# Kernel optimization log

Measured on AMD Instinct MI355X. Metric: run time of the kernel, lower is better.

## Reference

```python
import jax, jax.numpy as jnp
import numpy as np

N = 4096
C = 256
H = 8
D = C // H
E = 65536
MAX_DIST = 4
MAX_DEG = 32
FF_MULT = 2
EPS = 1e-5


def _layer_norm(x, gamma, beta):
    mu = jnp.mean(x, axis=-1, keepdims=True)
    var = jnp.mean(jnp.square(x - mu), axis=-1, keepdims=True)
    return (x - mu) * jax.lax.rsqrt(var + EPS) * gamma + beta


def _shortest_path_buckets(edge_index, num_nodes, max_distance):
    far = max_distance + 1
    row, col = edge_index[0], edge_index[1]
    adj = jnp.zeros((num_nodes, num_nodes), dtype=bool)
    adj = adj.at[row, col].set(True).at[col, row].set(True)
    ids = jnp.arange(num_nodes)
    dist = jnp.full((num_nodes, num_nodes), far, dtype=jnp.int32)
    dist = dist.at[ids, ids].set(0)
    seen = jnp.eye(num_nodes, dtype=bool)
    frontier = adj
    adj_i = adj.astype(jnp.int32)
    for d in range(1, max_distance + 1):  # small fixed loop (max_distance=4)
        frontier = frontier & ~seen
        dist = jnp.where(frontier, jnp.int32(d), dist)
        seen = seen | frontier
        frontier = (frontier.astype(jnp.int32) @ adj_i) > 0
    return dist


def setup_inputs() -> dict:
    key = jax.random.key(0)
    ks = jax.random.split(key, 16)
    s = 0.02
    inp = {
        'x': jax.random.normal(ks[0], (N, C), jnp.float32),
        'edge_index': jax.random.randint(ks[1], (2, E), 0, N, jnp.int64),
        'deg_emb': jax.random.normal(ks[2], (MAX_DEG + 2, C), jnp.float32) * s,
        'spa_emb': jax.random.normal(ks[3], (MAX_DIST + 2, H), jnp.float32) * s,
        'Wq': jax.random.normal(ks[4], (C, C), jnp.float32) * s,
        'bq': jnp.zeros((C,), jnp.float32),
        'Wk': jax.random.normal(ks[5], (C, C), jnp.float32) * s,
        'bk': jnp.zeros((C,), jnp.float32),
        'Wv': jax.random.normal(ks[6], (C, C), jnp.float32) * s,
        'bv': jnp.zeros((C,), jnp.float32),
        'Wo': jax.random.normal(ks[7], (C, C), jnp.float32) * s,
        'bo': jnp.zeros((C,), jnp.float32),
        'g1': jnp.ones((C,), jnp.float32),
        'b1': jnp.zeros((C,), jnp.float32),
        'g2': jnp.ones((C,), jnp.float32),
        'b2': jnp.zeros((C,), jnp.float32),
        'Wf1': jax.random.normal(ks[8], (C, FF_MULT * C), jnp.float32) * s,
        'bf1': jnp.zeros((FF_MULT * C,), jnp.float32),
        'Wf2': jax.random.normal(ks[9], (FF_MULT * C, C), jnp.float32) * s,
        'bf2': jnp.zeros((C,), jnp.float32),
    }
    return inp


def _forward(x, edge_index, deg_emb, spa_emb, Wq, bq, Wk, bk, Wv, bv, Wo, bo,
             g1, b1, g2, b2, Wf1, bf1, Wf2, bf2):
    num_nodes = x.shape[0]
    row, col = edge_index[0], edge_index[1]
    # degree: in+out degree, clamped to max_degree+1
    deg = jnp.zeros((num_nodes,), jnp.int32).at[row].add(1).at[col].add(1)
    deg = jnp.minimum(deg, MAX_DEG + 1)
    hidden = x + deg_emb[deg]
    q = (hidden @ Wq + bq).reshape(num_nodes, H, D)
    k = (hidden @ Wk + bk).reshape(num_nodes, H, D)
    v = (hidden @ Wv + bv).reshape(num_nodes, H, D)
    scores = jnp.einsum('nhd,mhd->hnm', q, k) / jnp.sqrt(jnp.float32(D))
    dist = _shortest_path_buckets(edge_index, num_nodes, MAX_DIST)  # [N, N] int
    bias = spa_emb[dist].transpose(2, 0, 1)  # [H, N, N]
    attn = jax.nn.softmax(scores + bias, axis=-1)
    attended = jnp.einsum('hnm,mhd->nhd', attn, v).reshape(num_nodes, C)
    attended = attended @ Wo + bo
    h = _layer_norm(x + attended, g1, b1)
    ff = jax.nn.gelu(h @ Wf1 + bf1, approximate=False) @ Wf2 + bf2
    return _layer_norm(h + ff, g2, b2)


def reference(x, edge_index, deg_emb, spa_emb, Wq, bq, Wk, bk, Wv, bv, Wo, bo,
              g1, b1, g2, b2, Wf1, bf1, Wf2, bf2):
    return _forward(x, edge_index, deg_emb, spa_emb, Wq, bq, Wk, bk, Wv, bv,
                    Wo, bo, g1, b1, g2, b2, Wf1, bf1, Wf2, bf2)
```

## Files before the change

kernel.cpp:

```cpp
#include <hip/hip_runtime.h>
#include <math.h>

#define NN 4096
#define CC 256
#define HH 8
#define DD 32
#define EE 65536

typedef unsigned short u16;
typedef unsigned int u32;
typedef unsigned long long u64;
typedef unsigned char u8;

typedef float f32x4 __attribute__((ext_vector_type(4)));
typedef __bf16 bf16x8 __attribute__((ext_vector_type(8)));

__device__ __forceinline__ u16 f2b(float f){
  u32 u = __float_as_uint(f);
  return (u16)((u + 0x7FFFu + ((u >> 16) & 1u)) >> 16);
}
__device__ __forceinline__ u32 pk2(float a, float b){
  u32 r; asm("v_cvt_pk_bf16_f32 %0,%1,%2" : "=v"(r) : "v"(a), "v"(b)); return r;
}

__global__ __launch_bounds__(256) void k_deg(const int* __restrict__ ei, int* __restrict__ deg){
  int e = blockIdx.x * 256 + threadIdx.x;
  if (e < EE){
    atomicAdd(&deg[ei[e]], 1);
    atomicAdd(&deg[ei[EE + e]], 1);
  }
}

__global__ __launch_bounds__(256) void k_scan(const int* __restrict__ deg, int* __restrict__ rowp,
                                              int* __restrict__ cur){
  __shared__ int part[256];
  int t = threadIdx.x;
  int local[16];
  int s = 0;
  #pragma unroll
  for (int i = 0; i < 16; i++){ local[i] = s; s += deg[t*16 + i]; }
  part[t] = s;
  __syncthreads();
  for (int off = 1; off < 256; off <<= 1){
    int v = (t >= off) ? part[t - off] : 0;
    __syncthreads();
    part[t] += v;
    __syncthreads();
  }
  int excl = (t == 0) ? 0 : part[t - 1];
  #pragma unroll
  for (int i = 0; i < 16; i++){ int v = excl + local[i]; rowp[t*16+i] = v; cur[t*16+i] = v; }
  if (t == 255) rowp[4096] = excl + s;
}

__global__ __launch_bounds__(256) void k_fill(const int* __restrict__ ei, int* __restrict__ cur,
                                              int* __restrict__ col){
  int e = blockIdx.x * 256 + threadIdx.x;
  if (e < EE){
    int r = ei[e], c = ei[EE + e];
    col[atomicAdd(&cur[r], 1)] = c;
    col[atomicAdd(&cur[c], 1)] = r;
  }
}

__global__ __launch_bounds__(256) void k_hidden(const float* __restrict__ x, const float* __restrict__ demb,
                                                const int* __restrict__ deg, u16* __restrict__ hb){
  int i = blockIdx.x * 256 + threadIdx.x;
  int n = i >> 8, c = i & 255;
  int d = deg[n]; if (d > 33) d = 33;
  hb[i] = f2b(x[i] + demb[d * CC + c]);
}

__global__ __launch_bounds__(256) void k_b0(u64* __restrict__ B0){
  int i = blockIdx.x * 256 + threadIdx.x;
  int j = i >> 6, w = i & 63;
  B0[i] = (w == (j >> 6)) ? (1ull << (j & 63)) : 0ull;
}

__global__ __launch_bounds__(256) void k_prop(const u64* __restrict__ Bp, u64* __restrict__ Bn,
                                              const int* __restrict__ rowp, const int* __restrict__ col){
  int i = blockIdx.x * 256 + threadIdx.x;
  int j = i >> 6, w = i & 63;
  u64 acc = Bp[i];
  int s = rowp[j], e = rowp[j + 1];
  u64 a0 = 0, a1 = 0, a2 = 0, a3 = 0;
  int p = s;
  for (; p + 4 <= e; p += 4){
    int c0 = col[p], c1 = col[p+1], c2 = col[p+2], c3 = col[p+3];
    a0 |= Bp[(c0 << 6) + w];
    a1 |= Bp[(c1 << 6) + w];
    a2 |= Bp[(c2 << 6) + w];
    a3 |= Bp[(c3 << 6) + w];
  }
  for (; p < e; p++) a0 |= Bp[(col[p] << 6) + w];
  Bn[i] = acc | (a0 | a1) | (a2 | a3);
}

__global__ __launch_bounds__(256) void k_dist(const u64* __restrict__ B1, const u64* __restrict__ B2,
                                              const u64* __restrict__ B3, const u64* __restrict__ B4,
                                              u8* __restrict__ dist){
  int i = blockIdx.x * 256 + threadIdx.x;
  int j = i >> 6, w = i & 63;
  u64 b1 = B1[i], b2 = B2[i], b3 = B3[i], b4 = B4[i];
  u32 ob[16];
  #pragma unroll
  for (int g = 0; g < 16; g++){
    u32 word = 0;
    #pragma unroll
    for (int q = 0; q < 4; q++){
      int bit = g * 4 + q;
      u32 d;
      if ((b1 >> bit) & 1) d = 1;
      else if ((b2 >> bit) & 1) d = 2;
      else if ((b3 >> bit) & 1) d = 3;
      else if ((b4 >> bit) & 1) d = 4;
      else d = 5;
      if ((w << 6) + bit == j) d = 0;
      word |= d << (q * 8);
    }
    ob[g] = word;
  }
  uint4* dp = (uint4*)(dist + ((size_t)j << 12) + (w << 6));
  uint4* ov = (uint4*)ob;
  dp[0] = ov[0]; dp[1] = ov[1]; dp[2] = ov[2]; dp[3] = ov[3];
}

__global__ __launch_bounds__(256) void k_tconv(const float* __restrict__ W0, const float* __restrict__ W1,
                                               const float* __restrict__ W2, const float* __restrict__ W3,
                                               const float* __restrict__ W4, const float* __restrict__ W5,
                                               u16* __restrict__ T0, u16* __restrict__ T1,
                                               u16* __restrict__ T2, u16* __restrict__ T3,
                                               u16* __restrict__ T4, u16* __restrict__ T5){
  __shared__ float Ts[64][65];
  int z = blockIdx.z;
  const float* W; u16* T; int K, N;
  switch (z){
    case 0: W = W0; T = T0; K = 256; N = 256; break;
    case 1: W = W1; T = T1; K = 256; N = 256; break;
    case 2: W = W2; T = T2; K = 256; N = 256; break;
    case 3: W = W3; T = T3; K = 256; N = 256; break;
    case 4: W = W4; T = T4; K = 256; N = 512; break;
    default: W = W5; T = T5; K = 512; N = 256; break;
  }
  int n0 = blockIdx.x * 64, k0 = blockIdx.y * 64;
  if (n0 >= N || k0 >= K) return;
  int t = threadIdx.x;
  int r = t >> 4, c4 = (t & 15) * 4;
  #pragma unroll
  for (int it = 0; it < 4; it++){
    float4 v = *(const float4*)&W[(size_t)(k0 + it*16 + r) * N + n0 + c4];
    Ts[it*16 + r][c4+0] = v.x; Ts[it*16 + r][c4+1] = v.y;
    Ts[it*16 + r][c4+2] = v.z; Ts[it*16 + r][c4+3] = v.w;
  }
  __syncthreads();
  #pragma unroll
  for (int it = 0; it < 4; it++){
    int n = it*16 + r;
    uint2 o;
    o.x = pk2(Ts[c4+0][n], Ts[c4+1][n]);
    o.y = pk2(Ts[c4+2][n], Ts[c4+3][n]);
    *(uint2*)&T[(size_t)(n0 + n) * K + k0 + c4] = o;
  }
}

__global__ __launch_bounds__(256) void k_bcat(const float* __restrict__ a, const float* __restrict__ b,
                                              const float* __restrict__ c, float* __restrict__ o){
  int i = blockIdx.x * 256 + threadIdx.x;
  if (i < 768){
    float v = (i < 256) ? a[i] : (i < 512) ? b[i - 256] : c[i - 512];
    o[i] = v;
  }
}

__global__ __launch_bounds__(256) void k_gemm32(const u16* __restrict__ A, const u16* __restrict__ Wt,
                                                const float* __restrict__ bias,
                                                float* __restrict__ outF, u16* __restrict__ outB,
                                                u16* __restrict__ outT,
                                                int M, int N, int K, int OS, int mode){
  __shared__ __align__(16) u16 As[32][72];
  __shared__ __align__(16) u16 Bs[64][72];
  int t = threadIdx.x;
  int lane = t & 63;
  int wv = t >> 6;
  int m0 = blockIdx.x * 32, n0 = blockIdx.y * 64;
  int ar = t >> 3, ak = (t & 7) * 8;
  int br = t >> 2, bk = (t & 3) * 16;
  int row16 = lane & 15, kq = (lane >> 4) * 8, rg = (lane >> 4) * 4;
  f32x4 acc0 = {0.f,0.f,0.f,0.f}, acc1 = {0.f,0.f,0.f,0.f};
  for (int k0 = 0; k0 < K; k0 += 64){
    __syncthreads();
    *(bf16x8*)&As[ar][ak]   = *(const bf16x8*)&A [(size_t)(m0 + ar) * K + k0 + ak];
    *(bf16x8*)&Bs[br][bk]   = *(const bf16x8*)&Wt[(size_t)(n0 + br) * K + k0 + bk];
    *(bf16x8*)&Bs[br][bk+8] = *(const bf16x8*)&Wt[(size_t)(n0 + br) * K + k0 + bk + 8];
    __syncthreads();
    #pragma unroll
    for (int ks = 0; ks < 2; ks++){
      bf16x8 a0 = *(const bf16x8*)&As[     row16][ks*32 + kq];
      bf16x8 a1 = *(const bf16x8*)&As[16 + row16][ks*32 + kq];
      bf16x8 b  = *(const bf16x8*)&Bs[wv*16 + row16][ks*32 + kq];
      acc0 = __builtin_amdgcn_mfma_f32_16x16x32_bf16(a0, b, acc0, 0, 0, 0);
      acc1 = __builtin_amdgcn_mfma_f32_16x16x32_bf16(a1, b, acc1, 0, 0, 0);
    }
  }
  int gn = n0 + wv*16 + row16;
  float bv = bias[gn];
  #pragma unroll
  for (int fm = 0; fm < 2; fm++){
    f32x4 aa = fm ? acc1 : acc0;
    #pragma unroll
    for (int r = 0; r < 4; r++){
      int gm = m0 + fm*16 + rg + r;
      float v = aa[r] + bv;
      if (mode & 8) v = 0.5f * v * (1.0f + erff(v * 0.70710678118654752f));
      if (outT && gn >= 512)      outT[(size_t)(gn - 512) * M + gm] = f2b(v);
      else if (mode & 1)          outF[(size_t)gm * N + gn] = v;
      else                        outB[(size_t)gm * OS + gn] = f2b(v);
    }
  }
}

__global__ __launch_bounds__(256) void k_attn(const u16* __restrict__ qg, const u16* __restrict__ kg,
                                              int CS, const u16* __restrict__ vtg,
                                              const u8* __restrict__ dist,
                                              const float* __restrict__ spa,
                                              float* __restrict__ pacc, float* __restrict__ pml){
  __shared__ __align__(16) u16 P[4][32][72];
  __shared__ __align__(16) u8 dls[4][32][72];
  __shared__ float spas[48];
  int t = threadIdx.x;
  int lane = t & 63;
  int wv = t >> 6;
  int h = blockIdx.y * 4 + wv;
  int q0 = blockIdx.x * 32;
  int ck = blockIdx.z;
  int kbase = ck * 1024;
  if (t < 48) spas[t] = spa[t] * 1.4426950408889634f;
  __syncthreads();
  int row16 = lane & 15;
  int kq = (lane >> 4) * 8;
  int rg = (lane >> 4) * 4;
  int hDD = h * DD;
  const char* spasB = (const char*)spas + (h << 2);
  int srow = lane >> 3, scol = (lane & 7) * 8;

  bf16x8 qf0 = *(const bf16x8*)&qg[(size_t)(q0 +      row16) * CS + hDD + kq];
  bf16x8 qf1 = *(const bf16x8*)&qg[(size_t)(q0 + 16 + row16) * CS + hDD + kq];

  const u16* kp0 = kg  + (size_t)(kbase +      row16) * CS + hDD + kq;
  const u16* kp1 = kg  + (size_t)(kbase + 16 + row16) * CS + hDD + kq;
  const u16* kp2 = kg  + (size_t)(kbase + 32 + row16) * CS + hDD + kq;
  const u16* kp3 = kg  + (size_t)(kbase + 48 + row16) * CS + hDD + kq;
  const u16* vp0 = vtg + (size_t)(hDD +      row16) * NN + kbase + kq;
  const u16* vp1 = vtg + (size_t)(hDD + 16 + row16) * NN + kbase + kq;
  const u8*  dp0 = dist + (size_t)(q0 +      srow) * NN + kbase + scol;
  const u8*  dp1 = dist + (size_t)(q0 +  8 + srow) * NN + kbase + scol;
  const u8*  dp2 = dist + (size_t)(q0 + 16 + srow) * NN + kbase + scol;
  const u8*  dp3 = dist + (size_t)(q0 + 24 + srow) * NN + kbase + scol;

  f32x4 zero = {0.f, 0.f, 0.f, 0.f};
  f32x4 acc[2][2] = {{zero, zero}, {zero, zero}};
  float ls[2] = {0.f, 0.f};
  const float scale2 = 0.25506600600499404f;

  uint2 dr0 = *(const uint2*)dp0; dp0 += 64;
  uint2 dr1 = *(const uint2*)dp1; dp1 += 64;
  uint2 dr2 = *(const uint2*)dp2; dp2 += 64;
  uint2 dr3 = *(const uint2*)dp3; dp3 += 64;

  for (int tt = 0; tt < 16; tt++){
    *(uint2*)&dls[wv][     srow][scol] = dr0;
    *(uint2*)&dls[wv][ 8 + srow][scol] = dr1;
    *(uint2*)&dls[wv][16 + srow][scol] = dr2;
    *(uint2*)&dls[wv][24 + srow][scol] = dr3;
    if (tt != 15){
      dr0 = *(const uint2*)dp0; dp0 += 64;
      dr1 = *(const uint2*)dp1; dp1 += 64;
      dr2 = *(const uint2*)dp2; dp2 += 64;
      dr3 = *(const uint2*)dp3; dp3 += 64;
    }
    bf16x8 kf0 = *(const bf16x8*)kp0; kp0 += 64 * 512;
    bf16x8 kf1 = *(const bf16x8*)kp1; kp1 += 64 * 512;
    bf16x8 kf2 = *(const bf16x8*)kp2; kp2 += 64 * 512;
    bf16x8 kf3 = *(const bf16x8*)kp3; kp3 += 64 * 512;
    f32x4 sc[2][4];
    sc[0][0] = __builtin_amdgcn_mfma_f32_16x16x32_bf16(kf0, qf0, zero, 0, 0, 0);
    sc[1][0] = __builtin_amdgcn_mfma_f32_16x16x32_bf16(kf0, qf1, zero, 0, 0, 0);
    sc[0][1] = __builtin_amdgcn_mfma_f32_16x16x32_bf16(kf1, qf0, zero, 0, 0, 0);
    sc[1][1] = __builtin_amdgcn_mfma_f32_16x16x32_bf16(kf1, qf1, zero, 0, 0, 0);
    sc[0][2] = __builtin_amdgcn_mfma_f32_16x16x32_bf16(kf2, qf0, zero, 0, 0, 0);
    sc[1][2] = __builtin_amdgcn_mfma_f32_16x16x32_bf16(kf2, qf1, zero, 0, 0, 0);
    sc[0][3] = __builtin_amdgcn_mfma_f32_16x16x32_bf16(kf3, qf0, zero, 0, 0, 0);
    sc[1][3] = __builtin_amdgcn_mfma_f32_16x16x32_bf16(kf3, qf1, zero, 0, 0, 0);
    #pragma unroll
    for (int fm = 0; fm < 2; fm++){
      int qrow = fm*16 + row16;
      float rs = 0.f;
      #pragma unroll
      for (int fn = 0; fn < 4; fn++){
        u32 dw5 = (*(const u32*)&dls[wv][qrow][fn*16 + rg]) << 5;
        float b0 = *(const float*)(spasB + (dw5 & 255u));
        float b1 = *(const float*)(spasB + ((dw5 >> 8) & 255u));
        float b2 = *(const float*)(spasB + ((dw5 >> 16) & 255u));
        float b3 = *(const float*)(spasB + (dw5 >> 24));
        float p0 = exp2f(fmaf(sc[fm][fn][0], scale2, b0));
        float p1 = exp2f(fmaf(sc[fm][fn][1], scale2, b1));
        float p2 = exp2f(fmaf(sc[fm][fn][2], scale2, b2));
        float p3 = exp2f(fmaf(sc[fm][fn][3], scale2, b3));
        rs += (p0 + p1) + (p2 + p3);
        uint2 pw = { pk2(p0, p1), pk2(p2, p3) };
        *(uint2*)&P[wv][qrow][fn*16 + rg] = pw;
      }
      ls[fm] += rs;
    }
    #pragma unroll
    for (int ks = 0; ks < 2; ks++){
      bf16x8 pa0 = *(const bf16x8*)&P[wv][     row16][ks*32 + kq];
      bf16x8 pa1 = *(const bf16x8*)&P[wv][16 + row16][ks*32 + kq];
      bf16x8 vf0 = *(const bf16x8*)(vp0 + ks*32);
      bf16x8 vf1 = *(const bf16x8*)(vp1 + ks*32);
      acc[0][0] = __builtin_amdgcn_mfma_f32_16x16x32_bf16(pa0, vf0, acc[0][0], 0, 0, 0);
      acc[0][1] = __builtin_amdgcn_mfma_f32_16x16x32_bf16(pa0, vf1, acc[0][1], 0, 0, 0);
      acc[1][0] = __builtin_amdgcn_mfma_f32_16x16x32_bf16(pa1, vf0, acc[1][0], 0, 0, 0);
      acc[1][1] = __builtin_amdgcn_mfma_f32_16x16x32_bf16(pa1, vf1, acc[1][1], 0, 0, 0);
    }
    vp0 += 64; vp1 += 64;
  }
  #pragma unroll
  for (int fm = 0; fm < 2; fm++){
    ls[fm] += __shfl_xor(ls[fm], 16, 64);
    ls[fm] += __shfl_xor(ls[fm], 32, 64);
  }
  size_t base = ((size_t)ck * 8 + h) * 4096 + q0;
  #pragma unroll
  for (int fm = 0; fm < 2; fm++)
    #pragma unroll
    for (int fd = 0; fd < 2; fd++)
      #pragma unroll
      for (int r = 0; r < 4; r++)
        pacc[(base + fm*16 + rg + r) * 32 + fd*16 + row16] = acc[fm][fd][r];
  if ((lane >> 4) == 0){
    #pragma unroll
    for (int fm = 0; fm < 2; fm++)
      pml[base + fm*16 + row16] = ls[fm];
  }
}

__global__ __launch_bounds__(256) void k_merge(const float* __restrict__ pacc,
                                               const float* __restrict__ pml,
                                               u16* __restrict__ attb){
  int row = blockIdx.x;
  int t = threadIdx.x;
  int h = t >> 5, col = t & 31;
  float o = 0.f, L = 0.f;
  #pragma unroll
  for (int c = 0; c < 4; c++){
    size_t base = ((size_t)c * 8 + h) * 4096 + row;
    o += pacc[base * 32 + col];
    L += pml[base];
  }
  attb[(size_t)row * 256 + h * 32 + col] = f2b(o / L);
}

__global__ __launch_bounds__(256) void k_ln(const float* __restrict__ ina, const float* __restrict__ inb,
                                            const float* __restrict__ g, const float* __restrict__ b,
                                            float* __restrict__ outF, u16* __restrict__ outB){
  int t = threadIdx.x;
  int wv = t >> 6, lane = t & 63;
  int row = blockIdx.x * 4 + wv;
  size_t base = (size_t)row * CC + lane * 4;
  float4 xa = *(const float4*)&ina[base];
  float4 xb = *(const float4*)&inb[base];
  float v0 = xa.x + xb.x, v1 = xa.y + xb.y, v2 = xa.z + xb.z, v3 = xa.w + xb.w;
  float s  = v0 + v1 + v2 + v3;
  float s2 = v0*v0 + v1*v1 + v2*v2 + v3*v3;
  #pragma unroll
  for (int m = 1; m < 64; m <<= 1){
    s  += __shfl_xor(s,  m, 64);
    s2 += __shfl_xor(s2, m, 64);
  }
  float mu  = s * (1.0f / 256.0f);
  float var = s2 * (1.0f / 256.0f) - mu * mu;
  float rs  = rsqrtf(var + 1e-5f);
  float4 gv = *(const float4*)&g[lane * 4];
  float4 bv = *(const float4*)&b[lane * 4];
  float o0 = (v0 - mu) * rs * gv.x + bv.x;
  float o1 = (v1 - mu) * rs * gv.y + bv.y;
  float o2 = (v2 - mu) * rs * gv.z + bv.z;
  float o3 = (v3 - mu) * rs * gv.w + bv.w;
  if (outF){ float4 o = {o0, o1, o2, o3}; *(float4*)&outF[base] = o; }
  if (outB){
    outB[base+0] = f2b(o0); outB[base+1] = f2b(o1);
    outB[base+2] = f2b(o2); outB[base+3] = f2b(o3);
  }
}

extern "C" void kernel_launch(void* const* d_in, const int* in_sizes, int n_in,
                              void* d_out, int out_size, void* d_ws, size_t ws_size,
                              hipStream_t stream){
  const float* x    = (const float*)d_in[0];
  const int*   ei   = (const int*)  d_in[1];
  const float* demb = (const float*)d_in[2];
  const float* spa  = (const float*)d_in[3];
  const float* Wq   = (const float*)d_in[4];
  const float* bq   = (const float*)d_in[5];
  const float* Wk   = (const float*)d_in[6];
  const float* bk   = (const float*)d_in[7];
  const float* Wv   = (const float*)d_in[8];
  const float* bv   = (const float*)d_in[9];
  const float* Wo   = (const float*)d_in[10];
  const float* bo   = (const float*)d_in[11];
  const float* g1   = (const float*)d_in[12];
  const float* b1   = (const float*)d_in[13];
  const float* g2   = (const float*)d_in[14];
  const float* b2   = (const float*)d_in[15];
  const float* Wf1  = (const float*)d_in[16];
  const float* bf1  = (const float*)d_in[17];
  const float* Wf2  = (const float*)d_in[18];
  const float* bf2  = (const float*)d_in[19];

  char* ws = (char*)d_ws;
  size_t off = 0;
  auto take = [&](size_t bytes)->char*{
    char* p = ws + off;
    off = (off + bytes + 255) & ~(size_t)255;
    return p;
  };
  int* deg    = (int*)take(4096 * 4);
  int* rowp   = (int*)take(4097 * 4);
  int* cur    = (int*)take(4096 * 4);
  int* col    = (int*)take(131072 * 4);
  u16* hid    = (u16*)take(2097152);
  u16* Wqkvt  = (u16*)take(768 * 256 * 2);
  u16* Wot    = (u16*)take(131072);
  u16* Wf1t   = (u16*)take(262144);
  u16* Wf2t   = (u16*)take(262144);
  float* bcat = (float*)take(768 * 4);
  u16* qkv    = (u16*)take(4194304);
  u16* vt     = (u16*)take(2097152);
  u16* attb   = (u16*)take(2097152);
  char* SC    = take(18 * 1048576);
  u8* dist    = (u8*)take(16777216);
  u64* B[5];
  for (int i = 0; i < 5; i++) B[i] = (u64*)(SC + (size_t)i * 2097152);
  float* pacc    = (float*)SC;
  float* pml     = (float*)(SC + 16777216);
  float* attnout = (float*)SC;
  float* hf      = (float*)(SC + 4194304);
  u16*   hbf     = (u16*)  (SC + 8388608);
  u16*   ff1     = (u16*)  dist;
  float* ff2     = (float*)(dist + 8388608);
  float* outp    = (float*)d_out;

  hipMemsetAsync(deg, 0, 4096 * 4, stream);
  k_deg   <<<256,  256, 0, stream>>>(ei, deg);
  k_scan  <<<1,    256, 0, stream>>>(deg, rowp, cur);
  k_fill  <<<256,  256, 0, stream>>>(ei, cur, col);
  k_hidden<<<4096, 256, 0, stream>>>(x, demb, deg, hid);
  k_b0    <<<1024, 256, 0, stream>>>(B[0]);
  for (int d = 0; d < 4; d++)
    k_prop<<<1024, 256, 0, stream>>>(B[d], B[d + 1], rowp, col);
  k_dist  <<<1024, 256, 0, stream>>>(B[1], B[2], B[3], B[4], dist);

  k_tconv<<<dim3(8, 8, 6), 256, 0, stream>>>(Wq, Wk, Wv, Wo, Wf1, Wf2,
                                             Wqkvt, Wqkvt + 256*256, Wqkvt + 512*256,
                                             Wot, Wf1t, Wf2t);
  k_bcat <<<3, 256, 0, stream>>>(bq, bk, bv, bcat);

  k_gemm32<<<dim3(128, 12), 256, 0, stream>>>(hid, Wqkvt, bcat, nullptr, qkv, vt,
                                              4096, 768, 256, 512, 2);

  k_attn <<<dim3(128, 2, 4), 256, 0, stream>>>(qkv, qkv + 256, 512, vt, dist, spa, pacc, pml);
  k_merge<<<4096, 256, 0, stream>>>(pacc, pml, attb);

  k_gemm32<<<dim3(128, 4), 256, 0, stream>>>(attb, Wot, bo, attnout, nullptr, nullptr,
                                             4096, 256, 256, 256, 1);
  k_ln   <<<1024, 256, 0, stream>>>(x, attnout, g1, b1, hf, hbf);
  k_gemm32<<<dim3(128, 8), 256, 0, stream>>>(hbf, Wf1t, bf1, nullptr, ff1, nullptr,
                                             4096, 512, 256, 512, 2 | 8);
  k_gemm32<<<dim3(128, 4), 256, 0, stream>>>(ff1, Wf2t, bf2, ff2, nullptr, nullptr,
                                             4096, 256, 512, 256, 1);
  k_ln   <<<1024, 256, 0, stream>>>(hf, ff2, g2, b2, outp, nullptr);
}
```

Before: 306.4 us.

## Fold softmax scale into Q, quantize spatial bias to bytes, split keys eight ways

```diff
diff --git a/kernel.cpp b/kernel.cpp
--- a/kernel.cpp
+++ b/kernel.cpp
@@ -18,6 +18,9 @@
 __device__ __forceinline__ u16 f2b(float f){
   u32 u = __float_as_uint(f);
   return (u16)((u + 0x7FFFu + ((u >> 16) & 1u)) >> 16);
+}
+__device__ __forceinline__ float b2f(u16 b){
+  return __uint_as_float(((u32)b) << 16);
 }
 __device__ __forceinline__ u32 pk2(float a, float b){
   u32 r; asm("v_cvt_pk_bf16_f32 %0,%1,%2" : "=v"(r) : "v"(a), "v"(b)); return r;
@@ -212,6 +215,7 @@
       int gm = m0 + fm*16 + rg + r;
       float v = aa[r] + bv;
       if (mode & 8) v = 0.5f * v * (1.0f + erff(v * 0.70710678118654752f));
+      if ((mode & 16) && gn < 256) v *= 0.25506600600499404f;
       if (outT && gn >= 512)      outT[(size_t)(gn - 512) * M + gm] = f2b(v);
       else if (mode & 1)          outF[(size_t)gm * N + gn] = v;
       else                        outB[(size_t)gm * OS + gn] = f2b(v);
@@ -223,25 +227,32 @@
                                               int CS, const u16* __restrict__ vtg,
                                               const u8* __restrict__ dist,
                                               const float* __restrict__ spa,
-                                              float* __restrict__ pacc, float* __restrict__ pml){
+                                              u16* __restrict__ pacc, float* __restrict__ pml){
   __shared__ __align__(16) u16 P[4][32][72];
   __shared__ __align__(16) u8 dls[4][32][72];
-  __shared__ float spas[48];
   int t = threadIdx.x;
   int lane = t & 63;
   int wv = t >> 6;
   int h = blockIdx.y * 4 + wv;
   int q0 = blockIdx.x * 32;
   int ck = blockIdx.z;
-  int kbase = ck * 1024;
-  if (t < 48) spas[t] = spa[t] * 1.4426950408889634f;
-  __syncthreads();
+  int kbase = ck * 512;
   int row16 = lane & 15;
   int kq = (lane >> 4) * 8;
   int rg = (lane >> 4) * 4;
   int hDD = h * DD;
-  const char* spasB = (const char*)spas + (h << 2);
   int srow = lane >> 3, scol = (lane & 7) * 8;
+
+  u32 ub[6];
+  #pragma unroll
+  for (int b = 0; b < 6; b++){
+    float f = fmaf(spa[b * 8 + h], 369.32993046f, 128.5f);
+    int ui = (int)f;
+    ui = ui < 0 ? 0 : (ui > 255 ? 255 : ui);
+    ub[b] = (u32)ui;
+  }
+  u32 B0123 = ub[0] | (ub[1] << 8) | (ub[2] << 16) | (ub[3] << 24);
+  u32 B45   = ub[4] | (ub[5] << 8);
 
   bf16x8 qf0 = *(const bf16x8*)&qg[(size_t)(q0 +      row16) * CS + hDD + kq];
   bf16x8 qf1 = *(const bf16x8*)&qg[(size_t)(q0 + 16 + row16) * CS + hDD + kq];
@@ -260,19 +271,18 @@
   f32x4 zero = {0.f, 0.f, 0.f, 0.f};
   f32x4 acc[2][2] = {{zero, zero}, {zero, zero}};
   float ls[2] = {0.f, 0.f};
-  const float scale2 = 0.25506600600499404f;
 
   uint2 dr0 = *(const uint2*)dp0; dp0 += 64;
   uint2 dr1 = *(const uint2*)dp1; dp1 += 64;
   uint2 dr2 = *(const uint2*)dp2; dp2 += 64;
   uint2 dr3 = *(const uint2*)dp3; dp3 += 64;
 
-  for (int tt = 0; tt < 16; tt++){
+  for (int tt = 0; tt < 8; tt++){
     *(uint2*)&dls[wv][     srow][scol] = dr0;
     *(uint2*)&dls[wv][ 8 + srow][scol] = dr1;
     *(uint2*)&dls[wv][16 + srow][scol] = dr2;
     *(uint2*)&dls[wv][24 + srow][scol] = dr3;
-    if (tt != 15){
+    if (tt != 7){
       dr0 = *(const uint2*)dp0; dp0 += 64;
       dr1 = *(const uint2*)dp1; dp1 += 64;
       dr2 = *(const uint2*)dp2; dp2 += 64;
@@ -297,15 +307,12 @@
       float rs = 0.f;
       #pragma unroll
       for (int fn = 0; fn < 4; fn++){
-        u32 dw5 = (*(const u32*)&dls[wv][qrow][fn*16 + rg]) << 5;
-        float b0 = *(const float*)(spasB + (dw5 & 255u));
-        float b1 = *(const float*)(spasB + ((dw5 >> 8) & 255u));
-        float b2 = *(const float*)(spasB + ((dw5 >> 16) & 255u));
-        float b3 = *(const float*)(spasB + (dw5 >> 24));
-        float p0 = exp2f(fmaf(sc[fm][fn][0], scale2, b0));
-        float p1 = exp2f(fmaf(sc[fm][fn][1], scale2, b1));
-        float p2 = exp2f(fmaf(sc[fm][fn][2], scale2, b2));
-        float p3 = exp2f(fmaf(sc[fm][fn][3], scale2, b3));
+        u32 dw = *(const u32*)&dls[wv][qrow][fn*16 + rg];
+        u32 pb = __builtin_amdgcn_perm(B45, B0123, dw);
+        float p0 = exp2f(fmaf((float)( pb        & 255u), 0.00390625f, sc[fm][fn][0]));
+        float p1 = exp2f(fmaf((float)((pb >>  8) & 255u), 0.00390625f, sc[fm][fn][1]));
+        float p2 = exp2f(fmaf((float)((pb >> 16) & 255u), 0.00390625f, sc[fm][fn][2]));
+        float p3 = exp2f(fmaf((float)( pb >> 24        ), 0.00390625f, sc[fm][fn][3]));
         rs += (p0 + p1) + (p2 + p3);
         uint2 pw = { pk2(p0, p1), pk2(p2, p3) };
         *(uint2*)&P[wv][qrow][fn*16 + rg] = pw;
@@ -337,7 +344,7 @@
     for (int fd = 0; fd < 2; fd++)
       #pragma unroll
       for (int r = 0; r < 4; r++)
-        pacc[(base + fm*16 + rg + r) * 32 + fd*16 + row16] = acc[fm][fd][r];
+        pacc[(base + fm*16 + rg + r) * 32 + fd*16 + row16] = f2b(acc[fm][fd][r]);
   if ((lane >> 4) == 0){
     #pragma unroll
     for (int fm = 0; fm < 2; fm++)
@@ -345,7 +352,7 @@
   }
 }
 
-__global__ __launch_bounds__(256) void k_merge(const float* __restrict__ pacc,
+__global__ __launch_bounds__(256) void k_merge(const u16* __restrict__ pacc,
                                                const float* __restrict__ pml,
                                                u16* __restrict__ attb){
   int row = blockIdx.x;
@@ -353,9 +360,9 @@
   int h = t >> 5, col = t & 31;
   float o = 0.f, L = 0.f;
   #pragma unroll
-  for (int c = 0; c < 4; c++){
+  for (int c = 0; c < 8; c++){
     size_t base = ((size_t)c * 8 + h) * 4096 + row;
-    o += pacc[base * 32 + col];
+    o += b2f(pacc[base * 32 + col]);
     L += pml[base];
   }
   attb[(size_t)row * 256 + h * 32 + col] = f2b(o / L);
@@ -442,7 +449,7 @@
   u8* dist    = (u8*)take(16777216);
   u64* B[5];
   for (int i = 0; i < 5; i++) B[i] = (u64*)(SC + (size_t)i * 2097152);
-  float* pacc    = (float*)SC;
+  u16*   pacc    = (u16*)SC;
   float* pml     = (float*)(SC + 16777216);
   float* attnout = (float*)SC;
   float* hf      = (float*)(SC + 4194304);
@@ -467,9 +474,9 @@
   k_bcat <<<3, 256, 0, stream>>>(bq, bk, bv, bcat);
 
   k_gemm32<<<dim3(128, 12), 256, 0, stream>>>(hid, Wqkvt, bcat, nullptr, qkv, vt,
-                                              4096, 768, 256, 512, 2);
-
-  k_attn <<<dim3(128, 2, 4), 256, 0, stream>>>(qkv, qkv + 256, 512, vt, dist, spa, pacc, pml);
+                                              4096, 768, 256, 512, 2 | 16);
+
+  k_attn <<<dim3(128, 2, 8), 256, 0, stream>>>(qkv, qkv + 256, 512, vt, dist, spa, pacc, pml);
   k_merge<<<4096, 256, 0, stream>>>(pacc, pml, attb);
 
   k_gemm32<<<dim3(128, 4), 256, 0, stream>>>(attb, Wot, bo, attnout, nullptr, nullptr,
```

After: 301.0 us. Within noise of the previous version (-1.8%).
